# Kernel optimization log

Hardware: AMD Instinct MI355X
Metric: run time of the kernel (lower is better)

The kernel has to match this reference:

```python
import jax, jax.numpy as jnp
import numpy as np

MIN_MZ, MAX_MZ, BIN_W = 0.0, 1000.0, 0.01
NUM_BINS = int((MAX_MZ - MIN_MZ) / BIN_W)      # 100000
GROUP, OUT_PER_GROUP = 30, 3
GROUPS = NUM_BINS // GROUP                      # 3333
BINNER_OUT = GROUPS * OUT_PER_GROUP             # 9999
SCALING = 0.5
EPS = 1e-6
B, P = 256, 512                                 # pairs, padded peaks per spectrum


def setup_inputs() -> dict:
    key = jax.random.key(0)
    ks = jax.random.split(key, 10)
    # mz drawn in [0, 1100): peaks >= max_mz are dropped by the range filter (ragged-like)
    mz = jax.random.uniform(ks[0], (B, 2, P), jnp.float32, 0.0, 1100.0)
    intensities = jax.random.uniform(ks[1], (B, 2, P), jnp.float32, 1e-3, 1.0)
    s = 0.02
    return dict(
        mz=mz,
        intensities=intensities,
        binner_w=jax.random.normal(ks[2], (GROUPS, GROUP, OUT_PER_GROUP), jnp.float32) * s,
        binner_b=jax.random.normal(ks[3], (GROUPS, OUT_PER_GROUP), jnp.float32) * s,
        w0=jax.random.normal(ks[4], (BINNER_OUT, 1000), jnp.float32) * s,
        b0=jnp.zeros((1000,), jnp.float32),
        w1=jax.random.normal(ks[5], (1000, 800), jnp.float32) * s,
        b1=jnp.zeros((800,), jnp.float32),
        w2=jax.random.normal(ks[6], (800, 800), jnp.float32) * s,
        b2=jnp.zeros((800,), jnp.float32),
        we=jax.random.normal(ks[7], (800, 400), jnp.float32) * s,
        be=jnp.zeros((400,), jnp.float32),
    )


def _bin_spectra(mz, inten):
    # mz, inten: [N, P] -> binned [N, NUM_BINS] via ragged scatter-add of inten**SCALING
    mzc = jax.lax.stop_gradient(mz)             # indices are non-differentiable
    mask = (mzc >= MIN_MZ) & (mzc < MAX_MZ)
    idx = jnp.clip(((mzc - MIN_MZ) / BIN_W).astype(jnp.int32), 0, NUM_BINS - 1)
    vals = jnp.where(mask, inten ** SCALING, 0.0)
    n = mz.shape[0]
    rows = jnp.arange(n)[:, None]               # [N,1] broadcast against [N,P]
    binned = jnp.zeros((n, NUM_BINS), jnp.float32)
    return binned.at[rows, idx].add(vals)


def _encoder(binned, binner_w, binner_b, w0, b0, w1, b1, w2, b2, we, be):
    n = binned.shape[0]
    # PeakBinner: block-diagonal micro-linears over groups of 30 bins (last 10 bins unused)
    xg = binned[:, : GROUPS * GROUP].reshape(n, GROUPS, GROUP)
    x = jnp.einsum('bgi,gio->bgo', xg, binner_w) + binner_b
    x = x.reshape(n, BINNER_OUT)
    x = jax.nn.relu(x @ w0 + b0)
    x = jax.nn.relu(x @ w1 + b1)                # dropout = identity at eval
    x = jax.nn.relu(x @ w2 + b2)
    return x @ we + be                           # [N, 400]


def reference(mz, intensities, binner_w, binner_b, w0, b0, w1, b1, w2, b2, we, be):
    bp = mz.shape[0]
    n = bp * 2
    binned = _bin_spectra(mz.reshape(n, P), intensities.reshape(n, P))
    emb = _encoder(binned, binner_w, binner_b, w0, b0, w1, b1, w2, b2, we, be)
    emb = emb.reshape(bp, 2, -1)
    e1, e2 = emb[:, 0], emb[:, 1]
    n1 = jnp.maximum(jnp.linalg.norm(e1, axis=1), EPS)
    n2 = jnp.maximum(jnp.linalg.norm(e2, axis=1), EPS)
    return jnp.sum(e1 * e2, axis=1) / (n1 * n2)  # [B] cosine similarity
```

## Files before the change

kernel.cpp:

```cpp
#include <hip/hip_runtime.h>

typedef __bf16 bf16;
typedef __bf16 bf16x8 __attribute__((ext_vector_type(8)));
typedef float  f32x4  __attribute__((ext_vector_type(4)));

#define NSPEC   512
#define BOUT    9999
#define K0A     10240
#define N00     1024
#define KSPLIT0 16

__device__ __forceinline__ void gload_lds16(const bf16* g, bf16* l) {
    auto* gp = reinterpret_cast<const __attribute__((address_space(1))) unsigned int*>(
        reinterpret_cast<uintptr_t>(g));
    auto* lp = reinterpret_cast<__attribute__((address_space(3))) unsigned int*>(
        reinterpret_cast<uintptr_t>(l));
    __builtin_amdgcn_global_load_lds(gp, lp, 16, 0, 0);
}

__device__ __forceinline__ void transpose_tile64(const float* __restrict__ src,
                                                 bf16* __restrict__ dst,
                                                 int K, int N, int K0,
                                                 float* tile, int bx, int by) {
    int n0 = bx * 64, k0 = by * 32;
    int t = threadIdx.x;
    {
        int kr = t >> 4, nc = (t & 15) * 4;
        int gk = k0 + kr;
#pragma unroll
        for (int e = 0; e < 4; ++e) {
            int gn = n0 + nc + e;
            tile[kr * 65 + nc + e] = (gk < K && gn < N) ? src[(size_t)gk * N + gn] : 0.0f;
        }
    }
    __syncthreads();
    {
        int nr = t >> 3, kc = (t & 7) * 4;
        bf16 v[4];
#pragma unroll
        for (int e = 0; e < 4; ++e) v[e] = (bf16)tile[(kc + e) * 65 + nr];
        *(ushort4*)&dst[(size_t)(n0 + nr) * K0 + k0 + kc] = *(ushort4*)v;
    }
}

__global__ __launch_bounds__(512) void prep_all(const float* __restrict__ mz,
                                                const float* __restrict__ inten,
                                                const float* __restrict__ bw,
                                                const float* __restrict__ bb,
                                                const float* __restrict__ w0,
                                                const float* __restrict__ w1,
                                                const float* __restrict__ w2,
                                                const float* __restrict__ we,
                                                bf16* __restrict__ A,
                                                bf16* __restrict__ B0t,
                                                bf16* __restrict__ B1t,
                                                bf16* __restrict__ B2t,
                                                bf16* __restrict__ BEt,
                                                bf16* __restrict__ H1b,
                                                bf16* __restrict__ H2b,
                                                float* __restrict__ psums) {
    __shared__ float smem[K0A];
    int b = blockIdx.x;
    if (b < 5120) {
        transpose_tile64(w0, B0t, BOUT, 1000, K0A, smem, b & 15, b >> 4);
    } else if (b < 5568) {
        int r = b - 5120;
        transpose_tile64(w1, B1t, 1000, 800, 1024, smem, r % 14, r / 14);
    } else if (b < 6016) {
        int r = b - 5568;
        transpose_tile64(w2, B2t, 800, 800, 1024, smem, r % 14, r / 14);
    } else if (b < 6240) {
        int r = b - 6016;
        transpose_tile64(we, BEt, 800, 400, 1024, smem, r % 7, r / 7);
    } else if (b < 6752) {
        const int spec = b - 6240;
        const int t = threadIdx.x;
#pragma unroll
        for (int i = 0; i < 5; ++i)
            *(float4*)&smem[(i * 512 + t) * 4] = float4{0.f, 0.f, 0.f, 0.f};
        __syncthreads();
        {
            float m = mz[(size_t)spec * 512 + t];
            float v = inten[(size_t)spec * 512 + t];
            bool mask = (m >= 0.0f) && (m < 1000.0f);
            int idx = (int)(m / 0.01f);
            idx = min(max(idx, 0), 99999);
            if (mask && idx < 99990) {
                int g = idx / 30;
                float val = sqrtf(v);
                const float* w = bw + (size_t)idx * 3;
                atomicAdd(&smem[g * 3 + 0], val * w[0]);
                atomicAdd(&smem[g * 3 + 1], val * w[1]);
                atomicAdd(&smem[g * 3 + 2], val * w[2]);
            }
        }
        __syncthreads();
        bf16* Arow = A + (size_t)spec * K0A;
#pragma unroll
        for (int i = 0; i < 5; ++i) {
            int c = (i * 512 + t) * 4;
            float4 s = *(const float4*)&smem[c];
            bf16 o[4];
            o[0] = (bf16)((c + 0 < BOUT) ? bb[c + 0] + s.x : 0.f);
            o[1] = (bf16)((c + 1 < BOUT) ? bb[c + 1] + s.y : 0.f);
            o[2] = (bf16)((c + 2 < BOUT) ? bb[c + 2] + s.z : 0.f);
            o[3] = (bf16)((c + 3 < BOUT) ? bb[c + 3] + s.w : 0.f);
            *(ushort4*)&Arow[c] = *(ushort4*)o;
        }
    } else if (b < 6784) {
        int idx = b - 6752;
        bf16* H = (idx < 16) ? H1b : H2b;
        int sub = idx & 15;
        int t = threadIdx.x;
        int row = sub * 32 + (t >> 4);
        int col = 896 + (t & 15) * 8;
        *(uint4*)&H[(size_t)row * 1024 + col] = uint4{0u, 0u, 0u, 0u};
    } else {
        for (int i = threadIdx.x; i < 768; i += 512) psums[i] = 0.f;
    }
}

__global__ __launch_bounds__(512) void gemm0_splitk(const bf16* __restrict__ A,
                                                    const bf16* __restrict__ Bt,
                                                    bf16* __restrict__ Cslab) {
    constexpr int K0 = K0A, KITERS = 10, BK = 64;
    __shared__ __align__(16) bf16 As[2][128 * BK];
    __shared__ __align__(16) bf16 Bs[2][128 * BK];
    const int bid = blockIdx.x;
    const int kp = bid & 15;
    const int tile = bid >> 4;
    const int mt = tile & 3, nt = tile >> 2;
    const int tid = threadIdx.x, wave = tid >> 6, lane = tid & 63;
    const int wm = wave & 1, wn = wave >> 1;
    const int lrow = lane & 15, quad = lane >> 4;

    const bf16* Ag = A  + (size_t)(mt * 128) * K0 + kp * (KITERS * BK);
    const bf16* Bg = Bt + (size_t)(nt * 128) * K0 + kp * (KITERS * BK);

    auto stage = [&](int buf, int kk) {
        const int k = kk * BK;
        const int lr = lane >> 3;
        const int lch = lane & 7;
#pragma unroll
        for (int j = 0; j < 2; ++j) {
            int row0 = j * 64 + wave * 8;
            int row = row0 + lr;
            int ch  = lch ^ (row & 7);
            gload_lds16(Ag + (size_t)row * K0 + k + ch * 8, &As[buf][row0 * BK]);
        }
#pragma unroll
        for (int j = 0; j < 2; ++j) {
            int row0 = j * 64 + wave * 8;
            int row = row0 + lr;
            int ch  = lch ^ (row & 7);
            gload_lds16(Bg + (size_t)row * K0 + k + ch * 8, &Bs[buf][row0 * BK]);
        }
    };

    f32x4 acc[4][2] = {};
    stage(0, 0);
    for (int kk = 0; kk < KITERS; ++kk) {
        const int cur = kk & 1;
        __syncthreads();
        if (kk + 1 < KITERS) stage(cur ^ 1, kk + 1);
#pragma unroll
        for (int ks = 0; ks < 2; ++ks) {
            bf16x8 af[4], bfr[2];
            const int c = ks * 4 + quad;
#pragma unroll
            for (int im = 0; im < 4; ++im) {
                int r = wm * 64 + im * 16 + lrow;
                af[im] = *(const bf16x8*)&As[cur][r * BK + ((c ^ (r & 7)) << 3)];
            }
#pragma unroll
            for (int in = 0; in < 2; ++in) {
                int r = wn * 32 + in * 16 + lrow;
                bfr[in] = *(const bf16x8*)&Bs[cur][r * BK + ((c ^ (r & 7)) << 3)];
            }
#pragma unroll
            for (int im = 0; im < 4; ++im)
#pragma unroll
                for (int in = 0; in < 2; ++in)
                    acc[im][in] = __builtin_amdgcn_mfma_f32_16x16x32_bf16(af[im], bfr[in], acc[im][in], 0, 0, 0);
        }
    }
    bf16* C = Cslab + (size_t)kp * (NSPEC * N00);
#pragma unroll
    for (int im = 0; im < 4; ++im) {
        int row0 = mt * 128 + wm * 64 + im * 16 + quad * 4;
#pragma unroll
        for (int in = 0; in < 2; ++in) {
            int col = nt * 128 + wn * 32 + in * 16 + lrow;
#pragma unroll
            for (int r = 0; r < 4; ++r)
                C[(size_t)(row0 + r) * N00 + col] = (bf16)acc[im][in][r];
        }
    }
}

__global__ __launch_bounds__(256) void reduce_bias_relu(const bf16* __restrict__ Cslab,
                                                        const float* __restrict__ b0,
                                                        bf16* __restrict__ H0b) {
    int idx = blockIdx.x * 256 + threadIdx.x;
    int r = idx >> 7, c = (idx & 127) * 8;
    float s[8] = {};
#pragma unroll
    for (int kp = 0; kp < KSPLIT0; ++kp) {
        bf16x8 v = *(const bf16x8*)&Cslab[(size_t)kp * (NSPEC * N00) + (size_t)r * N00 + c];
#pragma unroll
        for (int j = 0; j < 8; ++j) s[j] += (float)v[j];
    }
    bf16 o[8];
#pragma unroll
    for (int j = 0; j < 8; ++j)
        o[j] = (bf16)fmaxf(s[j] + ((c + j < 1000) ? b0[c + j] : 0.f), 0.f);
    *(uint4*)&H0b[(size_t)r * N00 + c] = *(uint4*)o;
}

template <bool LAST>
__global__ __launch_bounds__(512) void gemm_tail(const bf16* __restrict__ A,
                                                 const bf16* __restrict__ Bt,
                                                 const float* __restrict__ bias,
                                                 bf16* __restrict__ Ob,
                                                 float* __restrict__ psums,
                                                 int Nreal, int ntiles) {
    constexpr int BK = 256, KITERS = 4;
    __shared__ __align__(16) bf16 As[2][32 * BK];
    __shared__ __align__(16) bf16 Bs[2][32 * BK];
    __shared__ f32x4 xacc[4][64];
    const int bid = blockIdx.x;
    const int mt = bid / ntiles, nt = bid % ntiles;
    const int tid = threadIdx.x, wave = tid >> 6, lane = tid & 63;
    const int g = wave >> 2, w2 = wave & 3;
    const int wm = w2 & 1, wn = w2 >> 1;
    const int lrow = lane & 15, quad = lane >> 4;

    const bf16* Ag = A  + (size_t)(mt * 32) * 1024;
    const bf16* Bg = Bt + (size_t)(nt * 32) * 1024;

    auto stage = [&](int buf, int kk) {
        const int k = kk * BK;
#pragma unroll
        for (int j = 0; j < 2; ++j) {
            int row0 = (wave + j * 8) * 2;
            int row = row0 + (lane >> 5);
            int ch  = (lane & 31) ^ (row & 31);
            gload_lds16(Ag + (size_t)row * 1024 + k + ch * 8, &As[buf][row0 * BK]);
            gload_lds16(Bg + (size_t)row * 1024 + k + ch * 8, &Bs[buf][row0 * BK]);
        }
    };

    f32x4 acc = {};
    stage(0, 0);
    for (int kk = 0; kk < KITERS; ++kk) {
        const int cur = kk & 1;
        __syncthreads();
        if (kk + 1 < KITERS) stage(cur ^ 1, kk + 1);
#pragma unroll
        for (int ks = 0; ks < 4; ++ks) {
            int ra = wm * 16 + lrow, rb = wn * 16 + lrow;
            int c = g * 16 + ks * 4 + quad;
            bf16x8 af  = *(const bf16x8*)&As[cur][ra * BK + ((c ^ (ra & 31)) << 3)];
            bf16x8 bfr = *(const bf16x8*)&Bs[cur][rb * BK + ((c ^ (rb & 31)) << 3)];
            acc = __builtin_amdgcn_mfma_f32_16x16x32_bf16(af, bfr, acc, 0, 0, 0);
        }
    }
    __syncthreads();
    if (g == 1) xacc[w2][lane] = acc;
    __syncthreads();
    if (g == 0) {
        f32x4 o = xacc[w2][lane];
        acc[0] += o[0]; acc[1] += o[1]; acc[2] += o[2]; acc[3] += o[3];
        int row0 = mt * 32 + wm * 16 + quad * 4;
        int col  = nt * 32 + wn * 16 + lrow;
        if (!LAST) {
            float bv = (col < Nreal) ? bias[col] : 0.f;
#pragma unroll
            for (int r = 0; r < 4; ++r)
                Ob[(size_t)(row0 + r) * 1024 + col] = (bf16)fmaxf(acc[r] + bv, 0.f);
        } else {
            bool valid = (col < 400);
            float bv = valid ? bias[col] : 0.f;
            float v[4];
#pragma unroll
            for (int r = 0; r < 4; ++r) v[r] = valid ? (acc[r] + bv) : 0.f;
            int p0 = row0 >> 1;
            float sums[6] = {v[0] * v[1], v[0] * v[0], v[1] * v[1],
                             v[2] * v[3], v[2] * v[2], v[3] * v[3]};
#pragma unroll
            for (int off = 1; off < 16; off <<= 1)
#pragma unroll
                for (int s = 0; s < 6; ++s) sums[s] += __shfl_xor(sums[s], off);
            if (lrow == 0) {
#pragma unroll
                for (int s = 0; s < 3; ++s) {
                    atomicAdd(&psums[(p0 + 0) * 3 + s], sums[s]);
                    atomicAdd(&psums[(p0 + 1) * 3 + s], sums[3 + s]);
                }
            }
        }
    }
}

__global__ __launch_bounds__(256) void cosine_fin(const float* __restrict__ psums,
                                                  float* __restrict__ out) {
    int t = threadIdx.x;
    float d  = psums[t * 3 + 0];
    float s1 = psums[t * 3 + 1];
    float s2 = psums[t * 3 + 2];
    float n1 = fmaxf(sqrtf(s1), 1e-6f);
    float n2 = fmaxf(sqrtf(s2), 1e-6f);
    out[t] = d / (n1 * n2);
}

extern "C" void kernel_launch(void* const* d_in, const int* in_sizes, int n_in,
                              void* d_out, int out_size, void* d_ws, size_t ws_size,
                              hipStream_t stream) {
    const float* mz    = (const float*)d_in[0];
    const float* inten = (const float*)d_in[1];
    const float* bw    = (const float*)d_in[2];
    const float* bb    = (const float*)d_in[3];
    const float* w0    = (const float*)d_in[4];
    const float* b0    = (const float*)d_in[5];
    const float* w1    = (const float*)d_in[6];
    const float* b1    = (const float*)d_in[7];
    const float* w2    = (const float*)d_in[8];
    const float* b2    = (const float*)d_in[9];
    const float* we    = (const float*)d_in[10];
    const float* be    = (const float*)d_in[11];
    float* out = (float*)d_out;

    char* ws = (char*)d_ws;
    size_t off = 0;
    auto alloc = [&](size_t bytes) { char* p = ws + off; off += (bytes + 255) & ~(size_t)255; return p; };
    bf16*  A     = (bf16*) alloc((size_t)NSPEC * K0A * 2);
    bf16*  B0t   = (bf16*) alloc((size_t)N00 * K0A * 2);
    bf16*  B1t   = (bf16*) alloc((size_t)896 * 1024 * 2);
    bf16*  B2t   = (bf16*) alloc((size_t)896 * 1024 * 2);
    bf16*  BEt   = (bf16*) alloc((size_t)448 * 1024 * 2);
    bf16*  Cslab = (bf16*) alloc((size_t)KSPLIT0 * NSPEC * N00 * 2);
    bf16*  H0b   = (bf16*) alloc((size_t)NSPEC * 1024 * 2);
    bf16*  H1b   = (bf16*) alloc((size_t)NSPEC * 1024 * 2);
    bf16*  H2b   = (bf16*) alloc((size_t)NSPEC * 1024 * 2);
    float* psums = (float*)alloc(768 * 4);

    prep_all<<<6785, 512, 0, stream>>>(mz, inten, bw, bb, w0, w1, w2, we,
                                       A, B0t, B1t, B2t, BEt, H1b, H2b, psums);
    gemm0_splitk<<<512, 512, 0, stream>>>(A, B0t, Cslab);
    reduce_bias_relu<<<256, 256, 0, stream>>>(Cslab, b0, H0b);
    gemm_tail<false><<<448, 512, 0, stream>>>(H0b, B1t, b1, H1b, nullptr, 800, 28);
    gemm_tail<false><<<448, 512, 0, stream>>>(H1b, B2t, b2, H2b, nullptr, 800, 28);
    gemm_tail<true ><<<224, 512, 0, stream>>>(H2b, BEt, be, nullptr, psums, 400, 14);
    cosine_fin<<<1, 256, 0, stream>>>(psums, out);
}
```

Baseline: 163.4 us.

## Fuse encoder GEMM chain into one persistent kernel with grid barriers

Merges the split-K first GEMM, the reduction with bias and ReLU, the three tail GEMMs and the cosine finish into a single 512-block kernel. The phases are separated by atomic-counter grid barriers, and the counters are reset in the prep kernel. The aim is to remove five kernel launches and the gaps between them. The barriers only work if all 512 blocks are resident at once, which is why launch bounds request 4 blocks per CU. Spin-waiting and idle blocks in the smaller phases add their own cost.

After: 422.7 us. 2.59x slower.

```diff
diff --git a/kernel.cpp b/kernel.cpp
--- a/kernel.cpp
+++ b/kernel.cpp
@@ -9,6 +9,7 @@
 #define K0A     10240
 #define N00     1024
 #define KSPLIT0 16
+#define NBLK    512
 
 __device__ __forceinline__ void gload_lds16(const bf16* g, bf16* l) {
     auto* gp = reinterpret_cast<const __attribute__((address_space(1))) unsigned int*>(
@@ -16,6 +17,18 @@
     auto* lp = reinterpret_cast<__attribute__((address_space(3))) unsigned int*>(
         reinterpret_cast<uintptr_t>(l));
     __builtin_amdgcn_global_load_lds(gp, lp, 16, 0, 0);
+}
+
+__device__ __forceinline__ void grid_barrier(unsigned* bar) {
+    __syncthreads();
+    if (threadIdx.x == 0) {
+        __threadfence();
+        __hip_atomic_fetch_add(bar, 1u, __ATOMIC_ACQ_REL, __HIP_MEMORY_SCOPE_AGENT);
+        while (__hip_atomic_load(bar, __ATOMIC_RELAXED, __HIP_MEMORY_SCOPE_AGENT) < NBLK)
+            __builtin_amdgcn_s_sleep(8);
+        __threadfence();
+    }
+    __syncthreads();
 }
 
 __device__ __forceinline__ void transpose_tile64(const float* __restrict__ src,
@@ -58,7 +71,8 @@
                                                 bf16* __restrict__ BEt,
                                                 bf16* __restrict__ H1b,
                                                 bf16* __restrict__ H2b,
-                                                float* __restrict__ psums) {
+                                                float* __restrict__ psums,
+                                                unsigned* __restrict__ bars) {
     __shared__ float smem[K0A];
     int b = blockIdx.x;
     if (b < 5120) {
@@ -117,118 +131,20 @@
         *(uint4*)&H[(size_t)row * 1024 + col] = uint4{0u, 0u, 0u, 0u};
     } else {
         for (int i = threadIdx.x; i < 768; i += 512) psums[i] = 0.f;
-    }
-}
-
-__global__ __launch_bounds__(512) void gemm0_splitk(const bf16* __restrict__ A,
-                                                    const bf16* __restrict__ Bt,
-                                                    bf16* __restrict__ Cslab) {
-    constexpr int K0 = K0A, KITERS = 10, BK = 64;
-    __shared__ __align__(16) bf16 As[2][128 * BK];
-    __shared__ __align__(16) bf16 Bs[2][128 * BK];
-    const int bid = blockIdx.x;
-    const int kp = bid & 15;
-    const int tile = bid >> 4;
-    const int mt = tile & 3, nt = tile >> 2;
-    const int tid = threadIdx.x, wave = tid >> 6, lane = tid & 63;
-    const int wm = wave & 1, wn = wave >> 1;
-    const int lrow = lane & 15, quad = lane >> 4;
-
-    const bf16* Ag = A  + (size_t)(mt * 128) * K0 + kp * (KITERS * BK);
-    const bf16* Bg = Bt + (size_t)(nt * 128) * K0 + kp * (KITERS * BK);
-
-    auto stage = [&](int buf, int kk) {
-        const int k = kk * BK;
-        const int lr = lane >> 3;
-        const int lch = lane & 7;
-#pragma unroll
-        for (int j = 0; j < 2; ++j) {
-            int row0 = j * 64 + wave * 8;
-            int row = row0 + lr;
-            int ch  = lch ^ (row & 7);
-            gload_lds16(Ag + (size_t)row * K0 + k + ch * 8, &As[buf][row0 * BK]);
-        }
-#pragma unroll
-        for (int j = 0; j < 2; ++j) {
-            int row0 = j * 64 + wave * 8;
-            int row = row0 + lr;
-            int ch  = lch ^ (row & 7);
-            gload_lds16(Bg + (size_t)row * K0 + k + ch * 8, &Bs[buf][row0 * BK]);
-        }
-    };
-
-    f32x4 acc[4][2] = {};
-    stage(0, 0);
-    for (int kk = 0; kk < KITERS; ++kk) {
-        const int cur = kk & 1;
-        __syncthreads();
-        if (kk + 1 < KITERS) stage(cur ^ 1, kk + 1);
-#pragma unroll
-        for (int ks = 0; ks < 2; ++ks) {
-            bf16x8 af[4], bfr[2];
-            const int c = ks * 4 + quad;
-#pragma unroll
-            for (int im = 0; im < 4; ++im) {
-                int r = wm * 64 + im * 16 + lrow;
-                af[im] = *(const bf16x8*)&As[cur][r * BK + ((c ^ (r & 7)) << 3)];
-            }
-#pragma unroll
-            for (int in = 0; in < 2; ++in) {
-                int r = wn * 32 + in * 16 + lrow;
-                bfr[in] = *(const bf16x8*)&Bs[cur][r * BK + ((c ^ (r & 7)) << 3)];
-            }
-#pragma unroll
-            for (int im = 0; im < 4; ++im)
-#pragma unroll
-                for (int in = 0; in < 2; ++in)
-                    acc[im][in] = __builtin_amdgcn_mfma_f32_16x16x32_bf16(af[im], bfr[in], acc[im][in], 0, 0, 0);
-        }
-    }
-    bf16* C = Cslab + (size_t)kp * (NSPEC * N00);
-#pragma unroll
-    for (int im = 0; im < 4; ++im) {
-        int row0 = mt * 128 + wm * 64 + im * 16 + quad * 4;
-#pragma unroll
-        for (int in = 0; in < 2; ++in) {
-            int col = nt * 128 + wn * 32 + in * 16 + lrow;
-#pragma unroll
-            for (int r = 0; r < 4; ++r)
-                C[(size_t)(row0 + r) * N00 + col] = (bf16)acc[im][in][r];
-        }
-    }
-}
-
-__global__ __launch_bounds__(256) void reduce_bias_relu(const bf16* __restrict__ Cslab,
-                                                        const float* __restrict__ b0,
-                                                        bf16* __restrict__ H0b) {
-    int idx = blockIdx.x * 256 + threadIdx.x;
-    int r = idx >> 7, c = (idx & 127) * 8;
-    float s[8] = {};
-#pragma unroll
-    for (int kp = 0; kp < KSPLIT0; ++kp) {
-        bf16x8 v = *(const bf16x8*)&Cslab[(size_t)kp * (NSPEC * N00) + (size_t)r * N00 + c];
-#pragma unroll
-        for (int j = 0; j < 8; ++j) s[j] += (float)v[j];
-    }
-    bf16 o[8];
-#pragma unroll
-    for (int j = 0; j < 8; ++j)
-        o[j] = (bf16)fmaxf(s[j] + ((c + j < 1000) ? b0[c + j] : 0.f), 0.f);
-    *(uint4*)&H0b[(size_t)r * N00 + c] = *(uint4*)o;
+        if (threadIdx.x < 8) bars[threadIdx.x] = 0u;
+    }
 }
 
 template <bool LAST>
-__global__ __launch_bounds__(512) void gemm_tail(const bf16* __restrict__ A,
-                                                 const bf16* __restrict__ Bt,
-                                                 const float* __restrict__ bias,
-                                                 bf16* __restrict__ Ob,
-                                                 float* __restrict__ psums,
-                                                 int Nreal, int ntiles) {
+__device__ __forceinline__ void tail_phase(const bf16* __restrict__ A,
+                                           const bf16* __restrict__ Bt,
+                                           const float* __restrict__ bias,
+                                           bf16* __restrict__ Ob,
+                                           float* __restrict__ psums,
+                                           int Nreal, int ntiles, int bid,
+                                           bf16 (&As)[2][8192], bf16 (&Bs)[2][8192],
+                                           f32x4 (&xacc)[4][64]) {
     constexpr int BK = 256, KITERS = 4;
-    __shared__ __align__(16) bf16 As[2][32 * BK];
-    __shared__ __align__(16) bf16 Bs[2][32 * BK];
-    __shared__ f32x4 xacc[4][64];
-    const int bid = blockIdx.x;
     const int mt = bid / ntiles, nt = bid % ntiles;
     const int tid = threadIdx.x, wave = tid >> 6, lane = tid & 63;
     const int g = wave >> 2, w2 = wave & 3;
@@ -302,15 +218,139 @@
     }
 }
 
-__global__ __launch_bounds__(256) void cosine_fin(const float* __restrict__ psums,
-                                                  float* __restrict__ out) {
-    int t = threadIdx.x;
-    float d  = psums[t * 3 + 0];
-    float s1 = psums[t * 3 + 1];
-    float s2 = psums[t * 3 + 2];
-    float n1 = fmaxf(sqrtf(s1), 1e-6f);
-    float n2 = fmaxf(sqrtf(s2), 1e-6f);
-    out[t] = d / (n1 * n2);
+__global__ __launch_bounds__(512, 4) void encoder_fused(const bf16* __restrict__ A,
+                                                        const bf16* __restrict__ B0t,
+                                                        bf16* __restrict__ Cslab,
+                                                        const float* __restrict__ b0,
+                                                        bf16* __restrict__ H0b,
+                                                        const bf16* __restrict__ B1t,
+                                                        const float* __restrict__ b1,
+                                                        bf16* __restrict__ H1b,
+                                                        const bf16* __restrict__ B2t,
+                                                        const float* __restrict__ b2,
+                                                        bf16* __restrict__ H2b,
+                                                        const bf16* __restrict__ BEt,
+                                                        const float* __restrict__ be,
+                                                        float* __restrict__ psums,
+                                                        unsigned* __restrict__ bars,
+                                                        float* __restrict__ out) {
+    __shared__ __align__(16) bf16 As[2][8192];
+    __shared__ __align__(16) bf16 Bs[2][8192];
+    __shared__ f32x4 xacc[4][64];
+    const int bid = blockIdx.x;
+
+    {
+        constexpr int K0 = K0A, KITERS = 10, BK = 64;
+        const int kp = bid & 15;
+        const int tile = bid >> 4;
+        const int mt = tile & 3, nt = tile >> 2;
+        const int tid = threadIdx.x, wave = tid >> 6, lane = tid & 63;
+        const int wm = wave & 1, wn = wave >> 1;
+        const int lrow = lane & 15, quad = lane >> 4;
+
+        const bf16* Ag = A   + (size_t)(mt * 128) * K0 + kp * (KITERS * BK);
+        const bf16* Bg = B0t + (size_t)(nt * 128) * K0 + kp * (KITERS * BK);
+
+        auto stage = [&](int buf, int kk) {
+            const int k = kk * BK;
+            const int lr = lane >> 3;
+            const int lch = lane & 7;
+#pragma unroll
+            for (int j = 0; j < 2; ++j) {
+                int row0 = j * 64 + wave * 8;
+                int row = row0 + lr;
+                int ch  = lch ^ (row & 7);
+                gload_lds16(Ag + (size_t)row * K0 + k + ch * 8, &As[buf][row0 * BK]);
+            }
+#pragma unroll
+            for (int j = 0; j < 2; ++j) {
+                int row0 = j * 64 + wave * 8;
+                int row = row0 + lr;
+                int ch  = lch ^ (row & 7);
+                gload_lds16(Bg + (size_t)row * K0 + k + ch * 8, &Bs[buf][row0 * BK]);
+            }
+        };
+
+        f32x4 acc[4][2] = {};
+        stage(0, 0);
+        for (int kk = 0; kk < KITERS; ++kk) {
+            const int cur = kk & 1;
+            __syncthreads();
+            if (kk + 1 < KITERS) stage(cur ^ 1, kk + 1);
+#pragma unroll
+            for (int ks = 0; ks < 2; ++ks) {
+                bf16x8 af[4], bfr[2];
+                const int c = ks * 4 + quad;
+#pragma unroll
+                for (int im = 0; im < 4; ++im) {
+                    int r = wm * 64 + im * 16 + lrow;
+                    af[im] = *(const bf16x8*)&As[cur][r * BK + ((c ^ (r & 7)) << 3)];
+                }
+#pragma unroll
+                for (int in = 0; in < 2; ++in) {
+                    int r = wn * 32 + in * 16 + lrow;
+                    bfr[in] = *(const bf16x8*)&Bs[cur][r * BK + ((c ^ (r & 7)) << 3)];
+                }
+#pragma unroll
+                for (int im = 0; im < 4; ++im)
+#pragma unroll
+                    for (int in = 0; in < 2; ++in)
+                        acc[im][in] = __builtin_amdgcn_mfma_f32_16x16x32_bf16(af[im], bfr[in], acc[im][in], 0, 0, 0);
+            }
+        }
+        bf16* C = Cslab + (size_t)kp * (NSPEC * N00);
+#pragma unroll
+        for (int im = 0; im < 4; ++im) {
+            int row0 = mt * 128 + wm * 64 + im * 16 + quad * 4;
+#pragma unroll
+            for (int in = 0; in < 2; ++in) {
+                int col = nt * 128 + wn * 32 + in * 16 + lrow;
+#pragma unroll
+                for (int r = 0; r < 4; ++r)
+                    C[(size_t)(row0 + r) * N00 + col] = (bf16)acc[im][in][r];
+            }
+        }
+    }
+    grid_barrier(bars + 0);
+
+    {
+        int idx = bid * 512 + threadIdx.x;
+        if (idx < 65536) {
+            int r = idx >> 7, c = (idx & 127) * 8;
+            float s[8] = {};
+#pragma unroll
+            for (int kp = 0; kp < KSPLIT0; ++kp) {
+                bf16x8 v = *(const bf16x8*)&Cslab[(size_t)kp * (NSPEC * N00) + (size_t)r * N00 + c];
+#pragma unroll
+                for (int j = 0; j < 8; ++j) s[j] += (float)v[j];
+            }
+            bf16 o[8];
+#pragma unroll
+            for (int j = 0; j < 8; ++j)
+                o[j] = (bf16)fmaxf(s[j] + ((c + j < 1000) ? b0[c + j] : 0.f), 0.f);
+            *(uint4*)&H0b[(size_t)r * N00 + c] = *(uint4*)o;
+        }
+    }
+    grid_barrier(bars + 1);
+
+    if (bid < 448) tail_phase<false>(H0b, B1t, b1, H1b, nullptr, 800, 28, bid, As, Bs, xacc);
+    grid_barrier(bars + 2);
+
+    if (bid < 448) tail_phase<false>(H1b, B2t, b2, H2b, nullptr, 800, 28, bid, As, Bs, xacc);
+    grid_barrier(bars + 3);
+
+    if (bid < 224) tail_phase<true>(H2b, BEt, be, nullptr, psums, 400, 14, bid, As, Bs, xacc);
+    grid_barrier(bars + 4);
+
+    if (bid == 0 && threadIdx.x < 256) {
+        int t = threadIdx.x;
+        float d  = psums[t * 3 + 0];
+        float s1 = psums[t * 3 + 1];
+        float s2 = psums[t * 3 + 2];
+        float n1 = fmaxf(sqrtf(s1), 1e-6f);
+        float n2 = fmaxf(sqrtf(s2), 1e-6f);
+        out[t] = d / (n1 * n2);
+    }
 }
 
 extern "C" void kernel_launch(void* const* d_in, const int* in_sizes, int n_in,
@@ -343,13 +383,12 @@
     bf16*  H1b   = (bf16*) alloc((size_t)NSPEC * 1024 * 2);
     bf16*  H2b   = (bf16*) alloc((size_t)NSPEC * 1024 * 2);
     float* psums = (float*)alloc(768 * 4);
+    unsigned* bars = (unsigned*)alloc(8 * 4);
 
     prep_all<<<6785, 512, 0, stream>>>(mz, inten, bw, bb, w0, w1, w2, we,
-                                       A, B0t, B1t, B2t, BEt, H1b, H2b, psums);
-    gemm0_splitk<<<512, 512, 0, stream>>>(A, B0t, Cslab);
-    reduce_bias_relu<<<256, 256, 0, stream>>>(Cslab, b0, H0b);
-    gemm_tail<false><<<448, 512, 0, stream>>>(H0b, B1t, b1, H1b, nullptr, 800, 28);
-    gemm_tail<false><<<448, 512, 0, stream>>>(H1b, B2t, b2, H2b, nullptr, 800, 28);
-    gemm_tail<true ><<<224, 512, 0, stream>>>(H2b, BEt, be, nullptr, psums, 400, 14);
-    cosine_fin<<<1, 256, 0, stream>>>(psums, out);
-}
+                                       A, B0t, B1t, B2t, BEt, H1b, H2b, psums, bars);
+    encoder_fused<<<NBLK, 512, 0, stream>>>(A, B0t, Cslab, b0, H0b,
+                                            B1t, b1, H1b,
+                                            B2t, b2, H2b,
+                                            BEt, be, psums, bars, out);
+}
```
